# Optimization experiments

Measured on AMD Instinct MI355X. Metric: run time of the kernel, lower is better.

The kernel has to match this reference:

```python
import jax, jax.numpy as jnp
import numpy as np

V_MAX = 3.0
FEATURE_CLAMP = 10.0
TOP_K = 1


def _green_diag(d):
    """Diagonal of G = (tridiag(sub=1, diag=d, super=1))^{-1} for each batch row.
    d: (B, N) complex64. Stable two-sided continued-fraction (Thomas-like) recurrences:
      L_i = d_i - 1/L_{i-1},  U_i = d_i - 1/U_{i+1},  G_ii = 1/(L_i + U_i - d_i).
    Sequential over N (vectorized over B) via lax.scan.
    """
    dT = d.T  # (N, B)

    def step(c, di):
        nc = di - 1.0 / c
        return nc, nc

    L0 = dT[0]
    _, Lr = jax.lax.scan(step, L0, dT[1:])
    L = jnp.concatenate([L0[None], Lr], axis=0)  # (N, B)

    dR = dT[::-1]
    U0 = dR[0]
    _, Ur = jax.lax.scan(step, U0, dR[1:])
    U = jnp.concatenate([U0[None], Ur], axis=0)[::-1]  # (N, B)

    return (1.0 / (L + U - dT)).T  # (B, N)


def setup_inputs() -> dict:
    key = jax.random.key(0)
    B, N, D, E, F = 4, 4096, 512, 4, 2048
    ks = jax.random.split(key, 8)
    s = lambda k, sh, sc: (jax.random.normal(k, sh, jnp.float32) * sc)
    return dict(
        x=jax.random.normal(ks[0], (B, N, D), jnp.float32),
        v_proj_w=s(ks[1], (1, D), D ** -0.5),
        v_proj_b=jnp.zeros((1,), jnp.float32),
        gamma=jnp.float32(0.0),
        epsilon_param=jnp.float32(1.0),
        gate_w=s(ks[2], (E, D), D ** -0.5),
        gate_b=jnp.zeros((E,), jnp.float32),
        w1=s(ks[3], (E, D, F), D ** -0.5),
        b1=jnp.zeros((E, F), jnp.float32),
        w2=s(ks[4], (E, F, D), F ** -0.5),
        b2=jnp.zeros((E, D), jnp.float32),
        out_w=s(ks[5], (D, 2), 0.5),
        out_b=jnp.zeros((D,), jnp.float32),
        bk_scale=jnp.ones((D,), jnp.float32),
    )


def reference(x, v_proj_w, v_proj_b, gamma, epsilon_param, gate_w, gate_b,
              w1, b1, w2, b2, out_w, out_b, bk_scale):
    # 1) scalar potential from tokens
    v = jnp.einsum('bnd,od->bno', x, v_proj_w)[..., 0] + v_proj_b[0]  # (B, N)
    v = jnp.clip(v, -V_MAX, V_MAX)

    # 2) gamma-shifted complex tridiagonal Green's function diagonal
    eps = jax.nn.softplus(epsilon_param) + 1e-6
    z = 1j * (eps + gamma)                       # complex64 scalar
    d = ((v - 2.0).astype(jnp.complex64) - z)    # he_diag - z, (B, N)
    G = _green_diag(d)                            # (B, N) complex
    feats = jnp.clip(jnp.stack([G.real, G.imag], axis=-1), -FEATURE_CLAMP, FEATURE_CLAMP)  # (B,N,2)

    # 3) sparse MoE FFN (top-1 routing, experts = Linear -> GELU -> Linear)
    logits = jnp.einsum('bnd,ed->bne', x, gate_w) + gate_b
    probs = jax.nn.softmax(logits, axis=-1)
    top_p, top_i = jax.lax.top_k(probs, TOP_K)
    top_w = top_p / jnp.sum(top_p, axis=-1, keepdims=True)
    wmask = jnp.sum(jax.nn.one_hot(top_i, probs.shape[-1], dtype=probs.dtype) * top_w[..., None], axis=-2)  # (B,N,E)

    h = jax.nn.gelu(jnp.einsum('bnd,edf->benf', x, w1) + b1[None, :, None, :], approximate=False)
    y = jnp.einsum('benf,efd->bend', h, w2) + b2[None, :, None, :]
    ffn_out = jnp.einsum('bne,bend->bnd', wmask, y)

    # 4) combine spectral features with FFN output
    spec_out = jnp.einsum('bnc,dc->bnd', feats, out_w) + out_b
    return ffn_out + bk_scale * spec_out
```

## Files before the change

### kernel.cpp

```cpp
#include <hip/hip_runtime.h>
#include <hip/hip_bf16.h>
#include <math.h>


typedef __bf16 bf16x8 __attribute__((ext_vector_type(8)));
typedef float  f32x4  __attribute__((ext_vector_type(4)));
typedef __attribute__((address_space(3))) __bf16 lbf16;

#define B_   4
#define N_   4096
#define D_   512
#define E_   4
#define F_   2048
#define T_   (B_*N_)
#define CAP_ T_
#define R256 68
#define PADROWS (R256*256)

#define LGKM_BARRIER() asm volatile("s_waitcnt lgkmcnt(0)\n\ts_barrier" ::: "memory")

__device__ __forceinline__ void gload_lds16(const __bf16* g, lbf16* l) {
    __builtin_amdgcn_global_load_lds(
        (__attribute__((address_space(1))) void*)(void*)g,
        (__attribute__((address_space(3))) void*)l, 16, 0, 0);
}

__device__ __forceinline__ float fast_gelu(float x) {
    float u = 1.5957691216f * fmaf(0.044715f * x, x * x, x);
    return x / (1.0f + __expf(-u));
}

__device__ __forceinline__ void load8f2(const float2* p, float2* dst) {
    const float4* q = (const float4*)p;
    #pragma unroll
    for (int i = 0; i < 4; ++i) {
        float4 t = q[i];
        dst[2*i]   = make_float2(t.x, t.y);
        dst[2*i+1] = make_float2(t.z, t.w);
    }
}

__device__ __forceinline__ void mfma_tile(const char* Ab, const char* Bb,
                                          int cs0, int cs1, f32x4 acc[4][4]) {
    #pragma unroll
    for (int ks = 0; ks < 2; ++ks) {
        int cs = ks ? cs1 : cs0;
        bf16x8 af[4], bfr[4];
        #pragma unroll
        for (int m = 0; m < 4; ++m)
            af[m] = *(const bf16x8*)(Ab + m * 2048 + cs);
        #pragma unroll
        for (int n = 0; n < 4; ++n)
            bfr[n] = *(const bf16x8*)(Bb + n * 2048 + cs);
        #pragma unroll
        for (int m = 0; m < 4; ++m)
            #pragma unroll
            for (int n = 0; n < 4; ++n)
                acc[m][n] = __builtin_amdgcn_mfma_f32_16x16x32_bf16(af[m], bfr[n], acc[m][n], 0, 0, 0);
    }
}

__device__ alignas(256) __bf16 s_w1t[(size_t)E_*F_*D_];
__device__ alignas(256) __bf16 s_w2t[(size_t)E_*D_*F_];
__device__ alignas(256) __bf16 s_xb[(size_t)PADROWS*D_];
__device__ alignas(256) __bf16 s_H[(size_t)PADROWS*F_];
__device__ alignas(256) float2 s_d[T_];
__device__ alignas(256) float2 s_feats[T_];
__device__ alignas(256) float2 s_L[T_];
__device__ alignas(256) float2 s_U[T_];
__device__ alignas(256) int    s_perm[E_*CAP_];
__device__ alignas(256) int    s_cnt[E_];
__device__ alignas(256) int    s_tpre[8];
__device__ alignas(256) int    s_eid[T_];

__device__ inline float dot8(float4 a, float4 b, float4 c, float4 d) {
    float s =      a.x * c.x;
    s = fmaf(a.y, c.y, s); s = fmaf(a.z, c.z, s); s = fmaf(a.w, c.w, s);
    s = fmaf(b.x, d.x, s); s = fmaf(b.y, d.y, s); s = fmaf(b.z, d.z, s);
    s = fmaf(b.w, d.w, s);
    return s;
}

__device__ inline float wave_sum(float s) {
    #pragma unroll
    for (int off = 32; off > 0; off >>= 1) s += __shfl_xor(s, off);
    return s;
}

__global__ __launch_bounds__(256) void prep_trans_kernel(
        const float* __restrict__ w1, const float* __restrict__ w2,
        __bf16* __restrict__ w1t, __bf16* __restrict__ w2t,
        const float* __restrict__ x,
        const float* __restrict__ vw, const float* __restrict__ vb,
        const float* __restrict__ gamma, const float* __restrict__ epsp,
        const float* __restrict__ gw, const float* __restrict__ gb,
        float2* __restrict__ dbuf, int* __restrict__ eid) {
    __shared__ alignas(16) float tile[32][33];
    int idx = blockIdx.x;
    int tid = threadIdx.x;
    if (idx < 8192) {
        int which = idx >> 12;
        int r = idx & 4095;
        int e = r >> 10;
        int t = r & 1023;
        int R, C, c0, r0;
        const float* s;
        __bf16* d;
        if (which == 0) { R = D_; C = F_; c0 = (t & 63) * 32; r0 = (t >> 6) * 32;
                          s = w1 + (size_t)e * R * C; d = w1t + (size_t)e * R * C; }
        else            { R = F_; C = D_; c0 = (t & 15) * 32; r0 = (t >> 4) * 32;
                          s = w2 + (size_t)e * R * C; d = w2t + (size_t)e * R * C; }
        int tx = tid & 31, ty = tid >> 5;
        #pragma unroll
        for (int i = 0; i < 4; ++i)
            tile[ty + i*8][tx] = s[(size_t)(r0 + ty + i*8) * C + c0 + tx];
        __syncthreads();
        #pragma unroll
        for (int i = 0; i < 4; ++i)
            d[(size_t)(c0 + ty + i*8) * R + r0 + tx] = (__bf16)tile[tx][ty + i*8];
    } else {
        int wv = tid >> 6, lane = tid & 63;
        int token = (idx - 8192) * 4 + wv;
        const float4* xr = (const float4*)(x + (size_t)token * D_);
        float4 xa = xr[lane*2], xb = xr[lane*2 + 1];

        const float4* vr = (const float4*)vw;
        float sv = dot8(xa, xb, vr[lane*2], vr[lane*2 + 1]);
        float sg0, sg1, sg2, sg3;
        {
            const float4* g0 = (const float4*)(gw + 0*D_);
            const float4* g1 = (const float4*)(gw + 1*D_);
            const float4* g2 = (const float4*)(gw + 2*D_);
            const float4* g3 = (const float4*)(gw + 3*D_);
            sg0 = dot8(xa, xb, g0[lane*2], g0[lane*2+1]);
            sg1 = dot8(xa, xb, g1[lane*2], g1[lane*2+1]);
            sg2 = dot8(xa, xb, g2[lane*2], g2[lane*2+1]);
            sg3 = dot8(xa, xb, g3[lane*2], g3[lane*2+1]);
        }
        sv  = wave_sum(sv);
        sg0 = wave_sum(sg0); sg1 = wave_sum(sg1);
        sg2 = wave_sum(sg2); sg3 = wave_sum(sg3);

        if (lane == 0) {
            float v = sv + vb[0];
            v = fminf(fmaxf(v, -3.0f), 3.0f);
            float eps = log1pf(expf(epsp[0])) + 1e-6f;
            dbuf[token] = make_float2(v - 2.0f, -(eps + gamma[0]));

            float l0 = sg0 + gb[0], l1 = sg1 + gb[1], l2 = sg2 + gb[2], l3 = sg3 + gb[3];
            float best = l0; int be = 0;
            if (l1 > best) { best = l1; be = 1; }
            if (l2 > best) { best = l2; be = 2; }
            if (l3 > best) { best = l3; be = 3; }
            eid[token] = be;
        }
    }
}

__global__ __launch_bounds__(1024) void route_scan_kernel(
        const int* __restrict__ eid, int* __restrict__ perm,
        int* __restrict__ cnt, int* __restrict__ tpre,
        const float2* __restrict__ dbuf, float2* __restrict__ Lb,
        float2* __restrict__ Ub, float2* __restrict__ feats) {
    int tid = threadIdx.x;
    if (blockIdx.x == 0) {
        __shared__ int chunkcnt[256][4];
        __shared__ int chunkoff[256][4];
        __shared__ int totals[4];
        int wv = tid >> 6, lane = tid & 63;

        for (int c = wv; c < 256; c += 16) {
            int e = eid[c * 64 + lane];
            unsigned long long m0 = __ballot(e == 0);
            unsigned long long m1 = __ballot(e == 1);
            unsigned long long m2 = __ballot(e == 2);
            unsigned long long m3 = __ballot(e == 3);
            if (lane == 0) {
                chunkcnt[c][0] = __popcll(m0);
                chunkcnt[c][1] = __popcll(m1);
                chunkcnt[c][2] = __popcll(m2);
                chunkcnt[c][3] = __popcll(m3);
            }
        }
        __syncthreads();

        if (wv < 4) {
            int e = wv, carry = 0;
            #pragma unroll
            for (int g = 0; g < 4; ++g) {
                int idx = g * 64 + lane;
                int v = chunkcnt[idx][e];
                int s = v;
                #pragma unroll
                for (int off = 1; off < 64; off <<= 1) {
                    int u = __shfl_up(s, off);
                    if (lane >= off) s += u;
                }
                chunkoff[idx][e] = carry + s - v;
                carry += __shfl(s, 63);
            }
            if (lane == 0) { cnt[e] = carry; totals[e] = carry; }
        }
        __syncthreads();
        if (tid == 0) {
            int acc = 0;
            #pragma unroll
            for (int e = 0; e < E_; ++e) { tpre[e] = acc; acc += (totals[e] + 255) >> 8; }
            tpre[4] = acc;
        }

        for (int c = wv; c < 256; c += 16) {
            int t = c * 64 + lane;
            int e = eid[t];
            unsigned long long m0 = __ballot(e == 0);
            unsigned long long m1 = __ballot(e == 1);
            unsigned long long m2 = __ballot(e == 2);
            unsigned long long m3 = __ballot(e == 3);
            unsigned long long mym = (e == 0) ? m0 : (e == 1) ? m1 : (e == 2) ? m2 : m3;
            unsigned long long below = lane ? (mym & ((1ull << lane) - 1ull)) : 0ull;
            int pos = chunkoff[c][e] + __popcll(below);
            perm[e * CAP_ + pos] = t;
        }
    } else {
        __shared__ alignas(16) float chunkM[8][64][8];
        __shared__ alignas(16) float bound[8][64][4];
        int s = tid >> 6, c = tid & 63;
        int b = s & 3, dir = (s >> 2) & 1;

        if (tid < 512) {
            float ar=1, ai=0, br=0, bi=0, cr=0, ci=0, dr=1, di=0;
            float2 cur[8], nxt[8];
            {
                int seq0 = c * 64;
                const float2* p = dbuf + (dir ? (b*N_ + N_ - 8 - seq0) : (b*N_ + seq0));
                load8f2(p, cur);
            }
            for (int g = 0; g < 8; ++g) {
                if (g < 7) {
                    int seq0 = c * 64 + (g + 1) * 8;
                    const float2* p = dbuf + (dir ? (b*N_ + N_ - 8 - seq0) : (b*N_ + seq0));
                    load8f2(p, nxt);
                }
                #pragma unroll
                for (int q = 0; q < 8; ++q) {
                    float2 dv = dir ? cur[7 - q] : cur[q];
                    float nar = dv.x*ar - dv.y*ai - cr;
                    float nai = dv.x*ai + dv.y*ar - ci;
                    float nbr = dv.x*br - dv.y*bi - dr;
                    float nbi = dv.x*bi + dv.y*br - di;
                    cr = ar; ci = ai; dr = br; di = bi;
                    ar = nar; ai = nai; br = nbr; bi = nbi;
                }
                float m = fmaxf(fmaxf(fmaxf(fabsf(ar),fabsf(ai)),fmaxf(fabsf(br),fabsf(bi))),
                                fmaxf(fmaxf(fabsf(cr),fabsf(ci)),fmaxf(fabsf(dr),fabsf(di))));
                float inv = 1.0f / fmaxf(m, 1e-30f);
                ar*=inv; ai*=inv; br*=inv; bi*=inv; cr*=inv; ci*=inv; dr*=inv; di*=inv;
                #pragma unroll
                for (int q = 0; q < 8; ++q) cur[q] = nxt[q];
            }
            float* cm = chunkM[s][c];
            cm[0]=ar; cm[1]=ai; cm[2]=br; cm[3]=bi; cm[4]=cr; cm[5]=ci; cm[6]=dr; cm[7]=di;
        }
        __syncthreads();

        if (tid < 8) {
            int ss = tid;
            float pr=1, pi=0, qr=0, qi=0;
            for (int cc = 0; cc < 64; ++cc) {
                float* bd = bound[ss][cc];
                bd[0]=pr; bd[1]=pi; bd[2]=qr; bd[3]=qi;
                const float* m = chunkM[ss][cc];
                float npr = m[0]*pr - m[1]*pi + m[2]*qr - m[3]*qi;
                float npi = m[0]*pi + m[1]*pr + m[2]*qi + m[3]*qr;
                float nqr = m[4]*pr - m[5]*pi + m[6]*qr - m[7]*qi;
                float nqi = m[4]*pi + m[5]*pr + m[6]*qi + m[7]*qr;
                float mx = fmaxf(fmaxf(fabsf(npr),fabsf(npi)), fmaxf(fabsf(nqr),fabsf(nqi)));
                float inv = 1.0f / fmaxf(mx, 1e-30f);
                pr = npr*inv; pi = npi*inv; qr = nqr*inv; qi = nqi*inv;
            }
        }
        __syncthreads();

        if (tid < 512) {
            const float* bd = bound[s][c];
            float pr=bd[0], pi=bd[1], qr=bd[2], qi=bd[3];
            float den = fmaxf(pr*pr + pi*pi, 1e-30f);
            float invr = (qr*pr + qi*pi) / den;
            float invi = (qi*pr - qr*pi) / den;
            float2 cur[8], nxt[8];
            {
                int seq0 = c * 64;
                const float2* p = dbuf + (dir ? (b*N_ + N_ - 8 - seq0) : (b*N_ + seq0));
                load8f2(p, cur);
            }
            for (int g = 0; g < 8; ++g) {
                if (g < 7) {
                    int seq0 = c * 64 + (g + 1) * 8;
                    const float2* p = dbuf + (dir ? (b*N_ + N_ - 8 - seq0) : (b*N_ + seq0));
                    load8f2(p, nxt);
                }
                #pragma unroll
                for (int q = 0; q < 8; ++q) {
                    int seq = c * 64 + g * 8 + q;
                    int orig = dir ? (N_ - 1 - seq) : seq;
                    int t = b * N_ + orig;
                    float2 dv = dir ? cur[7 - q] : cur[q];
                    float Lr = dv.x - invr, Li = dv.y - invi;
                    if (dir) Ub[t] = make_float2(Lr, Li);
                    else     Lb[t] = make_float2(Lr, Li);
                    float d2 = Lr*Lr + Li*Li;
                    invr = Lr / d2; invi = -Li / d2;
                }
                #pragma unroll
                for (int q = 0; q < 8; ++q) cur[q] = nxt[q];
            }
        }
        __threadfence();
        __syncthreads();

        for (int t = tid; t < T_; t += 1024) {
            float2 L = Lb[t], U = Ub[t], dv = dbuf[t];
            float sr = L.x + U.x - dv.x;
            float si = L.y + U.y - dv.y;
            float den = sr*sr + si*si;
            float Gr = sr / den, Gi = -si / den;
            Gr = fminf(fmaxf(Gr, -10.0f), 10.0f);
            Gi = fminf(fmaxf(Gi, -10.0f), 10.0f);
            feats[t] = make_float2(Gr, Gi);
        }
    }
}

__global__ __launch_bounds__(256) void reorder_kernel(
        const float* __restrict__ x, const int* __restrict__ perm,
        const int* __restrict__ cnt, const int* __restrict__ tpre,
        __bf16* __restrict__ xb) {
    int wv = threadIdx.x >> 6, lane = threadIdx.x & 63;
    int prow = blockIdx.x * 4 + wv;
    if (prow >= tpre[4] * 256) return;
    int e = 0;
    #pragma unroll
    for (int k = 1; k < E_; ++k) if (prow >= tpre[k] * 256) e = k;
    int i = prow - tpre[e] * 256;
    int token = (i < cnt[e]) ? perm[e * CAP_ + i] : -1;
    bf16x8 v = {0,0,0,0,0,0,0,0};
    if (token >= 0) {
        const float4* xr = (const float4*)(x + (size_t)token * D_);
        float4 a = xr[lane*2], b = xr[lane*2 + 1];
        v = (bf16x8){(__bf16)a.x,(__bf16)a.y,(__bf16)a.z,(__bf16)a.w,
                     (__bf16)b.x,(__bf16)b.y,(__bf16)b.z,(__bf16)b.w};
    }
    *(bf16x8*)(xb + (size_t)prow * D_ + lane * 8) = v;
}

__global__ __launch_bounds__(512, 2) void gemm1_kernel(
        const __bf16* __restrict__ xb, const __bf16* __restrict__ w1t,
        const float* __restrict__ b1, __bf16* __restrict__ Hb,
        const int* __restrict__ tpre) {
    int bid = blockIdx.x;
    int lb  = (bid & 7) * 136 + (bid >> 3);
    int rt = lb >> 4, ct = lb & 15;
    if (rt >= tpre[4]) return;
    int e = 0;
    #pragma unroll
    for (int k = 1; k < E_; ++k) if (rt >= tpre[k]) e = k;

    extern __shared__ char smem[];
    char* Abase = smem;
    char* Bbase = smem + 65536;

    int tid = threadIdx.x, lane = tid & 63, wv = tid >> 6;
    int fl = lane & 15, gl = lane >> 4;
    int wr = wv >> 1, wc = wv & 1;

    int r8    = lane >> 3;
    int scolb = ((lane & 7) * 16) ^ (r8 << 4);
    const __bf16* aS0 = xb  + (size_t)(rt * 256 + wv * 32 + r8) * 512 + (scolb >> 1);
    const __bf16* bS0 = w1t + (size_t)(e * F_ + ct * 128 + wv * 16 + r8) * 512 + (scolb >> 1);
    lbf16* aD[2] = { (lbf16*)Abase + wv * 2048,
                     (lbf16*)(Abase + 32768) + wv * 2048 };
    lbf16* bD0   = (lbf16*)Bbase + wv * 1024;

    int xorv = (fl & 7) << 4;
    int cs0 = (gl * 16) ^ xorv;
    int cs1 = (64 + gl * 16) ^ xorv;
    const char* Ab[2] = { Abase + (wr * 64 + fl) * 128,
                          Abase + 32768 + (wr * 64 + fl) * 128 };
    const char* Bb = Bbase + (wc * 64 + fl) * 128;

    f32x4 acc[4][4];
    #pragma unroll
    for (int m = 0; m < 4; ++m)
        #pragma unroll
        for (int n = 0; n < 4; ++n) acc[m][n] = (f32x4){0.f,0.f,0.f,0.f};

    #pragma unroll
    for (int i = 0; i < 4; ++i)
        gload_lds16(aS0 + (size_t)i * 8 * 512, aD[0] + i * 512);
    #pragma unroll
    for (int i = 0; i < 2; ++i)
        gload_lds16(bS0 + (size_t)i * 8 * 512, bD0 + i * 512);

    for (int kt = 0; kt < 8; ++kt) {
        __syncthreads();
        int cur = kt & 1;
        if (kt + 1 < 8) {
            #pragma unroll
            for (int i = 0; i < 4; ++i)
                gload_lds16(aS0 + (size_t)i * 8 * 512 + (kt + 1) * 64, aD[cur ^ 1] + i * 512);
        }
        mfma_tile(Ab[cur], Bb, cs0, cs1, acc);
        if (kt + 1 < 8) {
            LGKM_BARRIER();
            #pragma unroll
            for (int i = 0; i < 2; ++i)
                gload_lds16(bS0 + (size_t)i * 8 * 512 + (kt + 1) * 64, bD0 + i * 512);
        }
    }

    int gre = rt * 256 + wr * 64;
    int gce = ct * 128 + wc * 64;
    float b1v[4];
    #pragma unroll
    for (int n = 0; n < 4; ++n) b1v[n] = b1[e * F_ + gce + n*16 + fl];
    #pragma unroll
    for (int m = 0; m < 4; ++m)
        #pragma unroll
        for (int r = 0; r < 4; ++r) {
            __bf16* hrow = Hb + (size_t)(gre + m*16 + gl*4 + r) * F_ + gce;
            #pragma unroll
            for (int n = 0; n < 4; ++n)
                hrow[n*16 + fl] = (__bf16)fast_gelu(acc[m][n][r] + b1v[n]);
        }
}

__global__ __launch_bounds__(512, 4) void gemm2_kernel(
        const __bf16* __restrict__ Hb, const __bf16* __restrict__ w2t,
        const float* __restrict__ b2, const float* __restrict__ outw,
        const float* __restrict__ outb, const float* __restrict__ bk,
        const float2* __restrict__ feats, const int* __restrict__ perm,
        const int* __restrict__ cnt_p, const int* __restrict__ tpre,
        float* __restrict__ out) {
    int bid = blockIdx.x;
    int lb  = (bid & 7) * 34 + (bid >> 3);
    int rt = lb >> 2, ct = lb & 3;
    if (rt >= tpre[4]) return;
    int e = 0;
    #pragma unroll
    for (int k = 1; k < E_; ++k) if (rt >= tpre[k]) e = k;

    __shared__ __bf16 A[256 * 64];
    __shared__ __bf16 Bm[128 * 64];

    int tid = threadIdx.x, lane = tid & 63, wv = tid >> 6;
    int fl = lane & 15, gl = lane >> 4;
    int wr = wv >> 1, wc = wv & 1;

    int r8    = lane >> 3;
    int scolb = ((lane & 7) * 16) ^ (r8 << 4);
    const __bf16* aS0 = Hb  + (size_t)(rt * 256 + wv * 32 + r8) * F_ + (scolb >> 1);
    const __bf16* bS0 = w2t + (size_t)(e * D_ + ct * 128 + wv * 16 + r8) * F_ + (scolb >> 1);
    lbf16* aD0 = (lbf16*)A  + wv * 32 * 64;
    lbf16* bD0 = (lbf16*)Bm + wv * 16 * 64;

    int xorv = (fl & 7) << 4;
    int cs0 = (gl * 16) ^ xorv;
    int cs1 = (64 + gl * 16) ^ xorv;
    const char* Ab = (const char*)A  + (wr * 64 + fl) * 128;
    const char* Bb = (const char*)Bm + (wc * 64 + fl) * 128;

    f32x4 acc[4][4];
    #pragma unroll
    for (int m = 0; m < 4; ++m)
        #pragma unroll
        for (int n = 0; n < 4; ++n) acc[m][n] = (f32x4){0.f,0.f,0.f,0.f};

    #pragma unroll
    for (int i = 0; i < 4; ++i)
        gload_lds16(aS0 + (size_t)i * 8 * F_, aD0 + i * 512);
    #pragma unroll
    for (int i = 0; i < 2; ++i)
        gload_lds16(bS0 + (size_t)i * 8 * F_, bD0 + i * 512);

    for (int kt = 0; kt < 32; ++kt) {
        __syncthreads();
        mfma_tile(Ab, Bb, cs0, cs1, acc);
        if (kt + 1 < 32) {
            LGKM_BARRIER();
            #pragma unroll
            for (int i = 0; i < 4; ++i)
                gload_lds16(aS0 + (size_t)i * 8 * F_ + (kt + 1) * 64, aD0 + i * 512);
            #pragma unroll
            for (int i = 0; i < 2; ++i)
                gload_lds16(bS0 + (size_t)i * 8 * F_ + (kt + 1) * 64, bD0 + i * 512);
        }
    }

    int cnt = cnt_p[e];
    int ibase = rt * 256 + wr * 64 - tpre[e] * 256;
    int gce = ct * 128 + wc * 64;
    float c_b2[4], c_o0[4], c_o1[4], c_ob[4], c_bk[4];
    #pragma unroll
    for (int n = 0; n < 4; ++n) {
        int dcol = gce + n*16 + fl;
        c_b2[n] = b2[e * D_ + dcol];
        c_o0[n] = outw[dcol * 2 + 0];
        c_o1[n] = outw[dcol * 2 + 1];
        c_ob[n] = outb[dcol];
        c_bk[n] = bk[dcol];
    }
    #pragma unroll
    for (int m = 0; m < 4; ++m)
        #pragma unroll
        for (int r = 0; r < 4; ++r) {
            int i = ibase + m*16 + gl*4 + r;
            if (i >= cnt) continue;
            int token = perm[e * CAP_ + i];
            float2 ft = feats[token];
            float* orow = out + (size_t)token * D_;
            #pragma unroll
            for (int n = 0; n < 4; ++n) {
                int dcol = gce + n*16 + fl;
                float spec = ft.x * c_o0[n] + ft.y * c_o1[n] + c_ob[n];
                orow[dcol] = acc[m][n][r] + c_b2[n] + c_bk[n] * spec;
            }
        }
}

extern "C" void kernel_launch(void* const* d_in, const int* in_sizes, int n_in,
                              void* d_out, int out_size, void* d_ws, size_t ws_size,
                              hipStream_t stream) {
    const float* x     = (const float*)d_in[0];
    const float* vpw   = (const float*)d_in[1];
    const float* vpb   = (const float*)d_in[2];
    const float* gamma = (const float*)d_in[3];
    const float* epsp  = (const float*)d_in[4];
    const float* gw    = (const float*)d_in[5];
    const float* gb    = (const float*)d_in[6];
    const float* w1    = (const float*)d_in[7];
    const float* b1    = (const float*)d_in[8];
    const float* w2    = (const float*)d_in[9];
    const float* b2    = (const float*)d_in[10];
    const float* ow    = (const float*)d_in[11];
    const float* ob    = (const float*)d_in[12];
    const float* bk    = (const float*)d_in[13];
    float* out = (float*)d_out;

    const size_t szW  = (size_t)E_ * F_ * D_ * sizeof(__bf16);
    const size_t szF2 = (size_t)T_ * sizeof(float2);
    const size_t szPm = (size_t)E_ * CAP_ * sizeof(int);
    const size_t szCt = 256;
    const size_t szXb = (size_t)PADROWS * D_ * sizeof(__bf16);
    const size_t szH  = (size_t)PADROWS * F_ * sizeof(__bf16);
    const size_t szEi = (size_t)T_ * sizeof(int);
    size_t need = 2*szW + 4*szF2 + szPm + 2*szCt + szXb + szH + szEi + 16*256;

    __bf16 *w1t, *w2t, *xbuf, *Hbuf; float2 *dbuf, *Lb, *Ub, *feats;
    int *perm, *cnt, *tpre, *eid;
    int use_ws = (d_ws != nullptr && ws_size >= need);
    if (use_ws) {
        size_t off = 0;
        auto carve = [&](size_t bytes) {
            void* p = (char*)d_ws + off;
            off += (bytes + 255) & ~(size_t)255;
            return p;
        };
        w1t   = (__bf16*)carve(szW);
        w2t   = (__bf16*)carve(szW);
        xbuf  = (__bf16*)carve(szXb);
        Hbuf  = (__bf16*)carve(szH);
        dbuf  = (float2*)carve(szF2);
        Lb    = (float2*)carve(szF2);
        Ub    = (float2*)carve(szF2);
        feats = (float2*)carve(szF2);
        perm  = (int*)   carve(szPm);
        cnt   = (int*)   carve(szCt);
        tpre  = (int*)   carve(szCt);
        eid   = (int*)   carve(szEi);
    } else {
        void* p;
        hipGetSymbolAddress(&p, HIP_SYMBOL(s_w1t));  w1t   = (__bf16*)p;
        hipGetSymbolAddress(&p, HIP_SYMBOL(s_w2t));  w2t   = (__bf16*)p;
        hipGetSymbolAddress(&p, HIP_SYMBOL(s_xb));   xbuf  = (__bf16*)p;
        hipGetSymbolAddress(&p, HIP_SYMBOL(s_H));    Hbuf  = (__bf16*)p;
        hipGetSymbolAddress(&p, HIP_SYMBOL(s_d));    dbuf  = (float2*)p;
        hipGetSymbolAddress(&p, HIP_SYMBOL(s_L));    Lb    = (float2*)p;
        hipGetSymbolAddress(&p, HIP_SYMBOL(s_U));    Ub    = (float2*)p;
        hipGetSymbolAddress(&p, HIP_SYMBOL(s_feats));feats = (float2*)p;
        hipGetSymbolAddress(&p, HIP_SYMBOL(s_perm)); perm  = (int*)p;
        hipGetSymbolAddress(&p, HIP_SYMBOL(s_cnt));  cnt   = (int*)p;
        hipGetSymbolAddress(&p, HIP_SYMBOL(s_tpre)); tpre  = (int*)p;
        hipGetSymbolAddress(&p, HIP_SYMBOL(s_eid));  eid   = (int*)p;
    }

    static int lds_attr_set = 0;
    if (!lds_attr_set) {
        hipFuncSetAttribute((const void*)gemm1_kernel,
                            hipFuncAttributeMaxDynamicSharedMemorySize, 81920);
        lds_attr_set = 1;
    }

    prep_trans_kernel<<<12288, 256, 0, stream>>>(w1, w2, w1t, w2t,
                                                 x, vpw, vpb, gamma, epsp, gw, gb,
                                                 dbuf, eid);
    route_scan_kernel<<<2, 1024, 0, stream>>>(eid, perm, cnt, tpre, dbuf, Lb, Ub, feats);
    reorder_kernel<<<PADROWS/4, 256, 0, stream>>>(x, perm, cnt, tpre, xbuf);
    gemm1_kernel<<<R256*16, 512, 81920, stream>>>(xbuf, w1t, b1, Hbuf, tpre);
    gemm2_kernel<<<R256*4, 512, 0, stream>>>(Hbuf, w2t, b2, ow, ob, bk,
                                             feats, perm, cnt, tpre, out);
}
```

Baseline: 215.4 us.

## Double-buffer B tile in gemm1 and interleave prefetch with MFMA halves

```diff
diff --git a/kernel.cpp b/kernel.cpp
--- a/kernel.cpp
+++ b/kernel.cpp
@@ -18,6 +18,7 @@
 #define PADROWS (R256*256)
 
 #define LGKM_BARRIER() asm volatile("s_waitcnt lgkmcnt(0)\n\ts_barrier" ::: "memory")
+#define VM0_BARRIER()  asm volatile("s_waitcnt vmcnt(0)\n\ts_barrier" ::: "memory")
 
 __device__ __forceinline__ void gload_lds16(const __bf16* g, lbf16* l) {
     __builtin_amdgcn_global_load_lds(
@@ -40,24 +41,26 @@
     }
 }
 
+__device__ __forceinline__ void mfma_half(const char* Ab, const char* Bb,
+                                          int cs, f32x4 acc[4][4]) {
+    bf16x8 af[4], bfr[4];
+    #pragma unroll
+    for (int m = 0; m < 4; ++m)
+        af[m] = *(const bf16x8*)(Ab + m * 2048 + cs);
+    #pragma unroll
+    for (int n = 0; n < 4; ++n)
+        bfr[n] = *(const bf16x8*)(Bb + n * 2048 + cs);
+    #pragma unroll
+    for (int m = 0; m < 4; ++m)
+        #pragma unroll
+        for (int n = 0; n < 4; ++n)
+            acc[m][n] = __builtin_amdgcn_mfma_f32_16x16x32_bf16(af[m], bfr[n], acc[m][n], 0, 0, 0);
+}
+
 __device__ __forceinline__ void mfma_tile(const char* Ab, const char* Bb,
                                           int cs0, int cs1, f32x4 acc[4][4]) {
-    #pragma unroll
-    for (int ks = 0; ks < 2; ++ks) {
-        int cs = ks ? cs1 : cs0;
-        bf16x8 af[4], bfr[4];
-        #pragma unroll
-        for (int m = 0; m < 4; ++m)
-            af[m] = *(const bf16x8*)(Ab + m * 2048 + cs);
-        #pragma unroll
-        for (int n = 0; n < 4; ++n)
-            bfr[n] = *(const bf16x8*)(Bb + n * 2048 + cs);
-        #pragma unroll
-        for (int m = 0; m < 4; ++m)
-            #pragma unroll
-            for (int n = 0; n < 4; ++n)
-                acc[m][n] = __builtin_amdgcn_mfma_f32_16x16x32_bf16(af[m], bfr[n], acc[m][n], 0, 0, 0);
-    }
+    mfma_half(Ab, Bb, cs0, acc);
+    mfma_half(Ab, Bb, cs1, acc);
 }
 
 __device__ alignas(256) __bf16 s_w1t[(size_t)E_*F_*D_];
@@ -366,8 +369,10 @@
     for (int k = 1; k < E_; ++k) if (rt >= tpre[k]) e = k;
 
     extern __shared__ char smem[];
-    char* Abase = smem;
-    char* Bbase = smem + 65536;
+    char* A0 = smem;
+    char* A1 = smem + 32768;
+    char* B0 = smem + 65536;
+    char* B1 = smem + 81920;
 
     int tid = threadIdx.x, lane = tid & 63, wv = tid >> 6;
     int fl = lane & 15, gl = lane >> 4;
@@ -377,16 +382,14 @@
     int scolb = ((lane & 7) * 16) ^ (r8 << 4);
     const __bf16* aS0 = xb  + (size_t)(rt * 256 + wv * 32 + r8) * 512 + (scolb >> 1);
     const __bf16* bS0 = w1t + (size_t)(e * F_ + ct * 128 + wv * 16 + r8) * 512 + (scolb >> 1);
-    lbf16* aD[2] = { (lbf16*)Abase + wv * 2048,
-                     (lbf16*)(Abase + 32768) + wv * 2048 };
-    lbf16* bD0   = (lbf16*)Bbase + wv * 1024;
+    lbf16* aD[2] = { (lbf16*)A0 + wv * 2048, (lbf16*)A1 + wv * 2048 };
+    lbf16* bD[2] = { (lbf16*)B0 + wv * 1024, (lbf16*)B1 + wv * 1024 };
 
     int xorv = (fl & 7) << 4;
     int cs0 = (gl * 16) ^ xorv;
     int cs1 = (64 + gl * 16) ^ xorv;
-    const char* Ab[2] = { Abase + (wr * 64 + fl) * 128,
-                          Abase + 32768 + (wr * 64 + fl) * 128 };
-    const char* Bb = Bbase + (wc * 64 + fl) * 128;
+    const char* Ab[2] = { A0 + (wr * 64 + fl) * 128, A1 + (wr * 64 + fl) * 128 };
+    const char* Bb[2] = { B0 + (wc * 64 + fl) * 128, B1 + (wc * 64 + fl) * 128 };
 
     f32x4 acc[4][4];
     #pragma unroll
@@ -399,23 +402,27 @@
         gload_lds16(aS0 + (size_t)i * 8 * 512, aD[0] + i * 512);
     #pragma unroll
     for (int i = 0; i < 2; ++i)
-        gload_lds16(bS0 + (size_t)i * 8 * 512, bD0 + i * 512);
-
+        gload_lds16(bS0 + (size_t)i * 8 * 512, bD[0] + i * 512);
+
+    #pragma unroll
     for (int kt = 0; kt < 8; ++kt) {
-        __syncthreads();
-        int cur = kt & 1;
+        int cur = kt & 1, nxt = cur ^ 1;
+        VM0_BARRIER();
+        __builtin_amdgcn_sched_barrier(0);
         if (kt + 1 < 8) {
             #pragma unroll
-            for (int i = 0; i < 4; ++i)
-                gload_lds16(aS0 + (size_t)i * 8 * 512 + (kt + 1) * 64, aD[cur ^ 1] + i * 512);
-        }
-        mfma_tile(Ab[cur], Bb, cs0, cs1, acc);
+            for (int i = 0; i < 2; ++i)
+                gload_lds16(aS0 + (size_t)i * 8 * 512 + (kt + 1) * 64, aD[nxt] + i * 512);
+            gload_lds16(bS0 + (kt + 1) * 64, bD[nxt]);
+        }
+        mfma_half(Ab[cur], Bb[cur], cs0, acc);
         if (kt + 1 < 8) {
-            LGKM_BARRIER();
-            #pragma unroll
-            for (int i = 0; i < 2; ++i)
-                gload_lds16(bS0 + (size_t)i * 8 * 512 + (kt + 1) * 64, bD0 + i * 512);
-        }
+            #pragma unroll
+            for (int i = 2; i < 4; ++i)
+                gload_lds16(aS0 + (size_t)i * 8 * 512 + (kt + 1) * 64, aD[nxt] + i * 512);
+            gload_lds16(bS0 + (size_t)8 * 512 + (kt + 1) * 64, bD[nxt] + 512);
+        }
+        mfma_half(Ab[cur], Bb[cur], cs1, acc);
     }
 
     int gre = rt * 256 + wr * 64;
@@ -596,7 +603,7 @@
     static int lds_attr_set = 0;
     if (!lds_attr_set) {
         hipFuncSetAttribute((const void*)gemm1_kernel,
-                            hipFuncAttributeMaxDynamicSharedMemorySize, 81920);
+                            hipFuncAttributeMaxDynamicSharedMemorySize, 98304);
         lds_attr_set = 1;
     }
 
@@ -605,7 +612,7 @@
                                                  dbuf, eid);
     route_scan_kernel<<<2, 1024, 0, stream>>>(eid, perm, cnt, tpre, dbuf, Lb, Ub, feats);
     reorder_kernel<<<PADROWS/4, 256, 0, stream>>>(x, perm, cnt, tpre, xbuf);
-    gemm1_kernel<<<R256*16, 512, 81920, stream>>>(xbuf, w1t, b1, Hbuf, tpre);
+    gemm1_kernel<<<R256*16, 512, 98304, stream>>>(xbuf, w1t, b1, Hbuf, tpre);
     gemm2_kernel<<<R256*4, 512, 0, stream>>>(Hbuf, w2t, b2, ow, ob, bk,
                                              feats, perm, cnt, tpre, out);
 }
```

After: 206.3 us. 1.04x faster.
